# Kernel optimization log

Measured on AMD Instinct MI355X. Metric: run time of the kernel, lower is better.

The kernel has to match this reference:

```python
import jax, jax.numpy as jnp
import numpy as np

N = 50000        # nodes
DEG = 16         # avg degree
E_RAND = N * DEG # random directed edges (before self-loops)
B = 4
F_IN = 64
F_OUT = 64


def _build_normalized_adjacency():
    """COO form of A_hat = D^{-1/2} (A + I) D^{-1/2} for a random sparse graph."""
    rng = np.random.default_rng(0)
    src = rng.integers(0, N, size=E_RAND)
    dst = rng.integers(0, N, size=E_RAND)
    rows = np.concatenate([src, np.arange(N)])  # add self-loops (A + I)
    cols = np.concatenate([dst, np.arange(N)])
    d = np.bincount(rows, minlength=N).astype(np.float32)  # row sums of A_tilde
    d_inv_sqrt = np.where(d > 0, 1.0 / np.sqrt(d), 0.0).astype(np.float32)
    vals = d_inv_sqrt[rows] * d_inv_sqrt[cols]
    return rows.astype(np.int32), cols.astype(np.int32), vals


def setup_inputs() -> dict:
    key = jax.random.key(0)
    k1, k2 = jax.random.split(key, 2)
    rows, cols, vals = _build_normalized_adjacency()
    x = jax.random.normal(k1, (B, N, F_IN), dtype=jnp.float32)
    # trunc_normal_(std=0.1) approximated by scaled normal
    weight = jax.random.normal(k2, (F_IN, F_OUT), dtype=jnp.float32) * 0.1
    bias = jnp.full((F_OUT,), 0.1, dtype=jnp.float32)
    return {
        "x": x,
        "vals": jnp.asarray(vals),
        "weight": weight,
        "bias": bias,
        "rows": jnp.asarray(rows),
        "cols": jnp.asarray(cols),
    }


def reference(x, vals, weight, bias, rows, cols):
    # SpMM: agg[b, r, f] = sum_e vals[e] * x[b, cols[e], f], scattered to rows[e]
    contrib = x[:, cols, :] * vals[None, :, None]          # [B, E, F_in]
    agg = jax.ops.segment_sum(contrib.transpose(1, 0, 2),  # [E, B, F_in]
                              rows, num_segments=N)        # [N, B, F_in]
    agg = agg.transpose(1, 0, 2)                           # [B, N, F_in]
    out = jnp.einsum('bnf,fo->bno', agg, weight) + bias    # dense GEMM + bias
    return jax.nn.elu(out)
```

## Files before the change

kernel.cpp:

```cpp
#include <hip/hip_runtime.h>
#include <math.h>

#define NNODES 50000
#define BB 4
#define FF 64
#define CAP 64

#define TROWS 32
#define GEMM_NB ((BB * NNODES) / TROWS)
#define RPB 4


__device__ inline unsigned short f2bf(float f) {
    unsigned u = __float_as_uint(f);
    u += 0x7fffu + ((u >> 16) & 1u);
    return (unsigned short)(u >> 16);
}

__device__ inline void bf4fma(float v, uint2 hv, float& a0, float& a1, float& a2, float& a3) {
    a0 = fmaf(v, __uint_as_float(hv.x << 16),         a0);
    a1 = fmaf(v, __uint_as_float(hv.x & 0xffff0000u), a1);
    a2 = fmaf(v, __uint_as_float(hv.y << 16),         a2);
    a3 = fmaf(v, __uint_as_float(hv.y & 0xffff0000u), a3);
}


__global__ __launch_bounds__(256) void prep_kernel(const int* __restrict__ rows,
                                                   const int* __restrict__ cols,
                                                   const float* __restrict__ vals,
                                                   int* __restrict__ cnt,
                                                   uint2* __restrict__ edata, int ES, int EPB,
                                                   int cstride,
                                                   const float* __restrict__ x,
                                                   const float* __restrict__ w,
                                                   unsigned short* __restrict__ h) {
    __shared__ float xs[TROWS][68];
    __shared__ float wsh[64][68];
    int t = threadIdx.x;
    long rowBase = (long)blockIdx.x * TROWS;

    #pragma unroll
    for (int i = 0; i < 2; ++i) {
        int s = t + i * 256;
        int r = s >> 4, c4 = s & 15;
        const float4* xp = (const float4*)(x + (rowBase + r) * 64 + c4 * 4);
        float4 xv;
        xv.x = __builtin_nontemporal_load(&xp->x);
        xv.y = __builtin_nontemporal_load(&xp->y);
        xv.z = __builtin_nontemporal_load(&xp->z);
        xv.w = __builtin_nontemporal_load(&xp->w);
        *(float4*)&xs[r][c4 * 4] = xv;
    }
    #pragma unroll
    for (int i = 0; i < 4; ++i) {
        int s = t + i * 256;
        int r = s >> 4, c4 = s & 15;
        *(float4*)&wsh[r][c4 * 4] = *(const float4*)(w + r * 64 + c4 * 4);
    }
    __syncthreads();

    int ty = t >> 4, tx = t & 15;
    int r0 = ty * 2, c0 = tx * 4;
    float acc[2][4] = {};
    #pragma unroll
    for (int f4 = 0; f4 < 16; ++f4) {
        float a[2][4], b[4][4];
        #pragma unroll
        for (int i = 0; i < 2; ++i)
            #pragma unroll
            for (int k = 0; k < 4; ++k) a[i][k] = xs[r0 + i][f4 * 4 + k];
        #pragma unroll
        for (int k = 0; k < 4; ++k)
            #pragma unroll
            for (int j = 0; j < 4; ++j) b[k][j] = wsh[f4 * 4 + k][c0 + j];
        #pragma unroll
        for (int i = 0; i < 2; ++i)
            #pragma unroll
            for (int k = 0; k < 4; ++k)
                #pragma unroll
                for (int j = 0; j < 4; ++j) acc[i][j] = fmaf(a[i][k], b[k][j], acc[i][j]);
    }
    #pragma unroll
    for (int i = 0; i < 2; ++i) {
        long m = rowBase + r0 + i;
        int  b = (int)(m / NNODES);
        int  n = (int)(m - (long)b * NNODES);
        ushort4 o;
        o.x = f2bf(acc[i][0]); o.y = f2bf(acc[i][1]);
        o.z = f2bf(acc[i][2]); o.w = f2bf(acc[i][3]);
        *(ushort4*)(h + ((size_t)n * BB + b) * 64 + c0) = o;
    }

    int e = blockIdx.x * EPB + t;
    if (t < EPB && e < ES) {
        int r = rows[e];
        int pos = atomicAdd(&cnt[(size_t)r * cstride], 1);
        if (pos < CAP)
            edata[(size_t)r * CAP + pos] = make_uint2((unsigned)cols[e], __float_as_uint(vals[e]));
    }
}


__global__ __launch_bounds__(256) void gather_kernel(const unsigned short* __restrict__ h,
                                                     const int* __restrict__ cnt,
                                                     const uint2* __restrict__ edata,
                                                     const float* __restrict__ vals,
                                                     const float* __restrict__ bias,
                                                     float* __restrict__ out,
                                                     int cstride, int ES) {
    int wave = threadIdx.x >> 6;
    int lane = threadIdx.x & 63;
    int r = blockIdx.x * RPB + wave;
    if (r >= NNODES) return;
    int deg = cnt[(size_t)r * cstride];
    if (deg > CAP) deg = CAP;
    int b  = lane >> 4;
    int fq = lane & 15;
    const unsigned short* hb = h + b * 64 + fq * 4;
    uint2 my_e = make_uint2(0u, 0u);
    if (lane < deg) {
        const uint2* ep = &edata[(size_t)r * CAP + lane];
        my_e.x = __builtin_nontemporal_load(&ep->x);
        my_e.y = __builtin_nontemporal_load(&ep->y);
    }
    int   my_c = (int)my_e.x;
    float my_v = __uint_as_float(my_e.y);
    float4 b4 = ((const float4*)bias)[fq];
    float a0 = 0.f, a1 = 0.f, a2 = 0.f, a3 = 0.f;
    int k = 0;
    for (; k + 8 <= deg; k += 8) {
        int   c0 = __shfl(my_c, k,     64), c1 = __shfl(my_c, k + 1, 64);
        int   c2 = __shfl(my_c, k + 2, 64), c3 = __shfl(my_c, k + 3, 64);
        int   c4 = __shfl(my_c, k + 4, 64), c5 = __shfl(my_c, k + 5, 64);
        int   c6 = __shfl(my_c, k + 6, 64), c7 = __shfl(my_c, k + 7, 64);
        float v0 = __shfl(my_v, k,     64), v1 = __shfl(my_v, k + 1, 64);
        float v2 = __shfl(my_v, k + 2, 64), v3 = __shfl(my_v, k + 3, 64);
        float v4 = __shfl(my_v, k + 4, 64), v5 = __shfl(my_v, k + 5, 64);
        float v6 = __shfl(my_v, k + 6, 64), v7 = __shfl(my_v, k + 7, 64);
        uint2 h0 = *(const uint2*)(hb + (size_t)(unsigned)c0 * 256);
        uint2 h1 = *(const uint2*)(hb + (size_t)(unsigned)c1 * 256);
        uint2 h2 = *(const uint2*)(hb + (size_t)(unsigned)c2 * 256);
        uint2 h3 = *(const uint2*)(hb + (size_t)(unsigned)c3 * 256);
        uint2 h4 = *(const uint2*)(hb + (size_t)(unsigned)c4 * 256);
        uint2 h5 = *(const uint2*)(hb + (size_t)(unsigned)c5 * 256);
        uint2 h6 = *(const uint2*)(hb + (size_t)(unsigned)c6 * 256);
        uint2 h7 = *(const uint2*)(hb + (size_t)(unsigned)c7 * 256);
        bf4fma(v0, h0, a0, a1, a2, a3);
        bf4fma(v1, h1, a0, a1, a2, a3);
        bf4fma(v2, h2, a0, a1, a2, a3);
        bf4fma(v3, h3, a0, a1, a2, a3);
        bf4fma(v4, h4, a0, a1, a2, a3);
        bf4fma(v5, h5, a0, a1, a2, a3);
        bf4fma(v6, h6, a0, a1, a2, a3);
        bf4fma(v7, h7, a0, a1, a2, a3);
    }
    for (; k + 4 <= deg; k += 4) {
        int   c0 = __shfl(my_c, k,     64), c1 = __shfl(my_c, k + 1, 64);
        int   c2 = __shfl(my_c, k + 2, 64), c3 = __shfl(my_c, k + 3, 64);
        float v0 = __shfl(my_v, k,     64), v1 = __shfl(my_v, k + 1, 64);
        float v2 = __shfl(my_v, k + 2, 64), v3 = __shfl(my_v, k + 3, 64);
        uint2 h0 = *(const uint2*)(hb + (size_t)(unsigned)c0 * 256);
        uint2 h1 = *(const uint2*)(hb + (size_t)(unsigned)c1 * 256);
        uint2 h2 = *(const uint2*)(hb + (size_t)(unsigned)c2 * 256);
        uint2 h3 = *(const uint2*)(hb + (size_t)(unsigned)c3 * 256);
        bf4fma(v0, h0, a0, a1, a2, a3);
        bf4fma(v1, h1, a0, a1, a2, a3);
        bf4fma(v2, h2, a0, a1, a2, a3);
        bf4fma(v3, h3, a0, a1, a2, a3);
    }
    for (; k < deg; ++k) {
        int   c = __shfl(my_c, k, 64);
        float v = __shfl(my_v, k, 64);
        uint2 hv = *(const uint2*)(hb + (size_t)(unsigned)c * 256);
        bf4fma(v, hv, a0, a1, a2, a3);
    }
    {
        float vs = vals[ES + r];
        uint2 hs = *(const uint2*)(hb + (size_t)r * 256);
        bf4fma(vs, hs, a0, a1, a2, a3);
    }
    a0 += b4.x; a1 += b4.y; a2 += b4.z; a3 += b4.w;
    a0 = a0 > 0.f ? a0 : expm1f(a0);
    a1 = a1 > 0.f ? a1 : expm1f(a1);
    a2 = a2 > 0.f ? a2 : expm1f(a2);
    a3 = a3 > 0.f ? a3 : expm1f(a3);
    float4 o = make_float4(a0, a1, a2, a3);
    *(float4*)(out + ((size_t)b * NNODES + r) * 64 + fq * 4) = o;
}


static inline size_t align256(size_t x) { return (x + 255) & ~(size_t)255; }

extern "C" void kernel_launch(void* const* d_in, const int* in_sizes, int n_in,
                              void* d_out, int out_size, void* d_ws, size_t ws_size,
                              hipStream_t stream) {
    const float* x    = (const float*)d_in[0];
    const float* vals = (const float*)d_in[1];
    const float* w    = (const float*)d_in[2];
    const float* bias = (const float*)d_in[3];
    const int*   rows = (const int*)d_in[4];
    const int*   cols = (const int*)d_in[5];
    float* out = (float*)d_out;
    const int E  = in_sizes[1];
    const int ES = E - NNODES;

    size_t h_b     = align256((size_t)BB * NNODES * FF * sizeof(unsigned short));
    size_t edata_b = align256((size_t)NNODES * CAP * sizeof(uint2));
    int cstride = 16;
    if (h_b + edata_b + align256((size_t)NNODES * 16 * sizeof(int)) > ws_size) cstride = 1;

    char* ws = (char*)d_ws;
    size_t off = 0;
    unsigned short* h = (unsigned short*)(ws + off);  off += h_b;
    int* cnt = (int*)(ws + off);
    off += align256((size_t)NNODES * cstride * sizeof(int));
    uint2* edata = (uint2*)(ws + off);                off += edata_b;

    int EPB = (ES + GEMM_NB - 1) / GEMM_NB;

    hipMemsetAsync(cnt, 0, (size_t)NNODES * cstride * sizeof(int), stream);
    prep_kernel<<<GEMM_NB, 256, 0, stream>>>(rows, cols, vals, cnt, edata, ES, EPB, cstride, x, w, h);
    gather_kernel<<<(NNODES + RPB - 1) / RPB, 256, 0, stream>>>(h, cnt, edata, vals, bias, out, cstride, ES);
}
```

Baseline: 112.2 us.

## Pack edge column and bf16 value into one word; pad gather loop to eight

Each edge record shrinks from a uint2 (int column plus fp32 value) to a single 32-bit word: the column goes in the low 16 bits and the bf16-rounded value in the high 16 bits. This halves edge-list write and read traffic and halves the shuffles per neighbour. The gather loop now rounds the degree up to a multiple of eight and drops the 4-wide and scalar tail loops; padded lanes read node 0 with weight zero. The self-loop value and feature load are also hoisted above the loop. In exchange, edge weights lose precision to bf16, and the packing only works while the node count stays below 65536.

```diff
diff --git a/kernel.cpp b/kernel.cpp
--- a/kernel.cpp
+++ b/kernel.cpp
@@ -29,7 +29,7 @@
                                                    const int* __restrict__ cols,
                                                    const float* __restrict__ vals,
                                                    int* __restrict__ cnt,
-                                                   uint2* __restrict__ edata, int ES, int EPB,
+                                                   unsigned* __restrict__ edata, int ES, int EPB,
                                                    int cstride,
                                                    const float* __restrict__ x,
                                                    const float* __restrict__ w,
@@ -95,15 +95,17 @@
     if (t < EPB && e < ES) {
         int r = rows[e];
         int pos = atomicAdd(&cnt[(size_t)r * cstride], 1);
-        if (pos < CAP)
-            edata[(size_t)r * CAP + pos] = make_uint2((unsigned)cols[e], __float_as_uint(vals[e]));
+        if (pos < CAP) {
+            unsigned p = ((unsigned)f2bf(vals[e]) << 16) | (unsigned)cols[e];
+            edata[(size_t)r * CAP + pos] = p;
+        }
     }
 }
 
 
 __global__ __launch_bounds__(256) void gather_kernel(const unsigned short* __restrict__ h,
                                                      const int* __restrict__ cnt,
-                                                     const uint2* __restrict__ edata,
+                                                     const unsigned* __restrict__ edata,
                                                      const float* __restrict__ vals,
                                                      const float* __restrict__ bias,
                                                      float* __restrict__ out,
@@ -117,68 +119,40 @@
     int b  = lane >> 4;
     int fq = lane & 15;
     const unsigned short* hb = h + b * 64 + fq * 4;
-    uint2 my_e = make_uint2(0u, 0u);
+    unsigned my_p = 0u;
     if (lane < deg) {
-        const uint2* ep = &edata[(size_t)r * CAP + lane];
-        my_e.x = __builtin_nontemporal_load(&ep->x);
-        my_e.y = __builtin_nontemporal_load(&ep->y);
+        const unsigned* ep = &edata[(size_t)r * CAP + lane];
+        my_p = __builtin_nontemporal_load(ep);
     }
-    int   my_c = (int)my_e.x;
-    float my_v = __uint_as_float(my_e.y);
+    float vs = vals[ES + r];
+    uint2 hs = *(const uint2*)(hb + (size_t)r * 256);
     float4 b4 = ((const float4*)bias)[fq];
+
     float a0 = 0.f, a1 = 0.f, a2 = 0.f, a3 = 0.f;
-    int k = 0;
-    for (; k + 8 <= deg; k += 8) {
-        int   c0 = __shfl(my_c, k,     64), c1 = __shfl(my_c, k + 1, 64);
-        int   c2 = __shfl(my_c, k + 2, 64), c3 = __shfl(my_c, k + 3, 64);
-        int   c4 = __shfl(my_c, k + 4, 64), c5 = __shfl(my_c, k + 5, 64);
-        int   c6 = __shfl(my_c, k + 6, 64), c7 = __shfl(my_c, k + 7, 64);
-        float v0 = __shfl(my_v, k,     64), v1 = __shfl(my_v, k + 1, 64);
-        float v2 = __shfl(my_v, k + 2, 64), v3 = __shfl(my_v, k + 3, 64);
-        float v4 = __shfl(my_v, k + 4, 64), v5 = __shfl(my_v, k + 5, 64);
-        float v6 = __shfl(my_v, k + 6, 64), v7 = __shfl(my_v, k + 7, 64);
-        uint2 h0 = *(const uint2*)(hb + (size_t)(unsigned)c0 * 256);
-        uint2 h1 = *(const uint2*)(hb + (size_t)(unsigned)c1 * 256);
-        uint2 h2 = *(const uint2*)(hb + (size_t)(unsigned)c2 * 256);
-        uint2 h3 = *(const uint2*)(hb + (size_t)(unsigned)c3 * 256);
-        uint2 h4 = *(const uint2*)(hb + (size_t)(unsigned)c4 * 256);
-        uint2 h5 = *(const uint2*)(hb + (size_t)(unsigned)c5 * 256);
-        uint2 h6 = *(const uint2*)(hb + (size_t)(unsigned)c6 * 256);
-        uint2 h7 = *(const uint2*)(hb + (size_t)(unsigned)c7 * 256);
-        bf4fma(v0, h0, a0, a1, a2, a3);
-        bf4fma(v1, h1, a0, a1, a2, a3);
-        bf4fma(v2, h2, a0, a1, a2, a3);
-        bf4fma(v3, h3, a0, a1, a2, a3);
-        bf4fma(v4, h4, a0, a1, a2, a3);
-        bf4fma(v5, h5, a0, a1, a2, a3);
-        bf4fma(v6, h6, a0, a1, a2, a3);
-        bf4fma(v7, h7, a0, a1, a2, a3);
+    int dg8 = (deg + 7) & ~7;
+    for (int k = 0; k < dg8; k += 8) {
+        unsigned p0 = __shfl(my_p, k,     64), p1 = __shfl(my_p, k + 1, 64);
+        unsigned p2 = __shfl(my_p, k + 2, 64), p3 = __shfl(my_p, k + 3, 64);
+        unsigned p4 = __shfl(my_p, k + 4, 64), p5 = __shfl(my_p, k + 5, 64);
+        unsigned p6 = __shfl(my_p, k + 6, 64), p7 = __shfl(my_p, k + 7, 64);
+        uint2 h0 = *(const uint2*)(hb + (size_t)(p0 & 0xFFFFu) * 256);
+        uint2 h1 = *(const uint2*)(hb + (size_t)(p1 & 0xFFFFu) * 256);
+        uint2 h2 = *(const uint2*)(hb + (size_t)(p2 & 0xFFFFu) * 256);
+        uint2 h3 = *(const uint2*)(hb + (size_t)(p3 & 0xFFFFu) * 256);
+        uint2 h4 = *(const uint2*)(hb + (size_t)(p4 & 0xFFFFu) * 256);
+        uint2 h5 = *(const uint2*)(hb + (size_t)(p5 & 0xFFFFu) * 256);
+        uint2 h6 = *(const uint2*)(hb + (size_t)(p6 & 0xFFFFu) * 256);
+        uint2 h7 = *(const uint2*)(hb + (size_t)(p7 & 0xFFFFu) * 256);
+        bf4fma(__uint_as_float(p0 & 0xFFFF0000u), h0, a0, a1, a2, a3);
+        bf4fma(__uint_as_float(p1 & 0xFFFF0000u), h1, a0, a1, a2, a3);
+        bf4fma(__uint_as_float(p2 & 0xFFFF0000u), h2, a0, a1, a2, a3);
+        bf4fma(__uint_as_float(p3 & 0xFFFF0000u), h3, a0, a1, a2, a3);
+        bf4fma(__uint_as_float(p4 & 0xFFFF0000u), h4, a0, a1, a2, a3);
+        bf4fma(__uint_as_float(p5 & 0xFFFF0000u), h5, a0, a1, a2, a3);
+        bf4fma(__uint_as_float(p6 & 0xFFFF0000u), h6, a0, a1, a2, a3);
+        bf4fma(__uint_as_float(p7 & 0xFFFF0000u), h7, a0, a1, a2, a3);
     }
-    for (; k + 4 <= deg; k += 4) {
-        int   c0 = __shfl(my_c, k,     64), c1 = __shfl(my_c, k + 1, 64);
-        int   c2 = __shfl(my_c, k + 2, 64), c3 = __shfl(my_c, k + 3, 64);
-        float v0 = __shfl(my_v, k,     64), v1 = __shfl(my_v, k + 1, 64);
-        float v2 = __shfl(my_v, k + 2, 64), v3 = __shfl(my_v, k + 3, 64);
-        uint2 h0 = *(const uint2*)(hb + (size_t)(unsigned)c0 * 256);
-        uint2 h1 = *(const uint2*)(hb + (size_t)(unsigned)c1 * 256);
-        uint2 h2 = *(const uint2*)(hb + (size_t)(unsigned)c2 * 256);
-        uint2 h3 = *(const uint2*)(hb + (size_t)(unsigned)c3 * 256);
-        bf4fma(v0, h0, a0, a1, a2, a3);
-        bf4fma(v1, h1, a0, a1, a2, a3);
-        bf4fma(v2, h2, a0, a1, a2, a3);
-        bf4fma(v3, h3, a0, a1, a2, a3);
-    }
-    for (; k < deg; ++k) {
-        int   c = __shfl(my_c, k, 64);
-        float v = __shfl(my_v, k, 64);
-        uint2 hv = *(const uint2*)(hb + (size_t)(unsigned)c * 256);
-        bf4fma(v, hv, a0, a1, a2, a3);
-    }
-    {
-        float vs = vals[ES + r];
-        uint2 hs = *(const uint2*)(hb + (size_t)r * 256);
-        bf4fma(vs, hs, a0, a1, a2, a3);
-    }
+    bf4fma(vs, hs, a0, a1, a2, a3);
     a0 += b4.x; a1 += b4.y; a2 += b4.z; a3 += b4.w;
     a0 = a0 > 0.f ? a0 : expm1f(a0);
     a1 = a1 > 0.f ? a1 : expm1f(a1);
@@ -205,7 +179,7 @@
     const int ES = E - NNODES;
 
     size_t h_b     = align256((size_t)BB * NNODES * FF * sizeof(unsigned short));
-    size_t edata_b = align256((size_t)NNODES * CAP * sizeof(uint2));
+    size_t edata_b = align256((size_t)NNODES * CAP * sizeof(unsigned));
     int cstride = 16;
     if (h_b + edata_b + align256((size_t)NNODES * 16 * sizeof(int)) > ws_size) cstride = 1;
 
@@ -214,7 +188,7 @@
     unsigned short* h = (unsigned short*)(ws + off);  off += h_b;
     int* cnt = (int*)(ws + off);
     off += align256((size_t)NNODES * cstride * sizeof(int));
-    uint2* edata = (uint2*)(ws + off);                off += edata_b;
+    unsigned* edata = (unsigned*)(ws + off);          off += edata_b;
 
     int EPB = (ES + GEMM_NB - 1) / GEMM_NB;
 
```

New measurement: 110.9 us. Within noise of the previous version (-1.1%).
